# Performance work log

Measured on AMD Instinct MI355X. Metric: run time of the kernel, lower is better.

Reference implementation:

```python
import jax, jax.numpy as jnp
import numpy as np

N_NODES = 50000
IN_CH, HID_CH, OUT_CH = 128, 128, 64
N_EDGES = 800000


def setup_inputs() -> dict:
    key = jax.random.key(0)
    k = jax.random.split(key, 6)
    x = jax.random.normal(k[0], (N_NODES, IN_CH), dtype=jnp.float32)
    edge_index = jax.random.randint(k[1], (2, N_EDGES), 0, N_NODES, dtype=jnp.int64)
    # Glorot-ish init for weights
    W1 = jax.random.normal(k[2], (IN_CH, HID_CH), dtype=jnp.float32) * (1.0 / np.sqrt(IN_CH))
    b1 = jnp.zeros((HID_CH,), dtype=jnp.float32)
    W2 = jax.random.normal(k[3], (HID_CH, OUT_CH), dtype=jnp.float32) * (1.0 / np.sqrt(HID_CH))
    b2 = jnp.zeros((OUT_CH,), dtype=jnp.float32)
    return {"x": x, "edge_index": edge_index, "W1": W1, "b1": b1, "W2": W2, "b2": b2}


def _gcn_conv(x, src, dst, W, b, n_nodes):
    """PyG GCNConv: linear, add self-loops, symmetric deg^-1/2 normalization, scatter-add."""
    h = x @ W  # [N, F_out]
    loop = jnp.arange(n_nodes, dtype=src.dtype)
    s = jnp.concatenate([src, loop])  # [E+N]
    d = jnp.concatenate([dst, loop])
    # in-degree on target nodes (including self-loops), edge weight = 1
    deg = jnp.zeros((n_nodes,), dtype=h.dtype).at[d].add(1.0)
    dinv = jnp.where(deg > 0, jax.lax.rsqrt(deg), 0.0)
    norm = dinv[s] * dinv[d]  # [E+N]
    msg = h[s] * norm[:, None]  # [E+N, F_out]
    out = jax.ops.segment_sum(msg, d, num_segments=n_nodes)
    return out + b


def reference(x, edge_index, W1, b1, W2, b2):
    src, dst = edge_index[0], edge_index[1]
    h = _gcn_conv(x, src, dst, W1, b1, N_NODES)
    h = jax.nn.relu(h)
    # dropout in eval mode -> identity
    out = _gcn_conv(h, src, dst, W2, b2, N_NODES)
    return out
```

## Files before the change

### kernel.cpp

```cpp
#include <hip/hip_runtime.h>

typedef __attribute__((ext_vector_type(8))) short bf16x8;
typedef __attribute__((ext_vector_type(4))) float f32x4;

constexpr int NN = 50000;
constexpr int NE = 800000;
constexpr int C1 = 128;
constexpr int C2 = 64;
constexpr int NBK = 196;
constexpr int EPB = 2048;
constexpr int NBLK = (NE + EPB - 1) / EPB;
constexpr int MT = NN / 16;
constexpr int MMB = 250;
constexpr int MMWAVES = MMB * 4;

__device__ __forceinline__ unsigned short f2bf(float f) {
    unsigned int u = __float_as_uint(f);
    u += 0x7FFFu + ((u >> 16) & 1u);
    return (unsigned short)(u >> 16);
}
__device__ __forceinline__ float2 bf2f(unsigned int u) {
    return make_float2(__uint_as_float(u << 16), __uint_as_float(u & 0xFFFF0000u));
}
__device__ __forceinline__ bf16x8 pack8(float4 a, float4 b) {
    bf16x8 r;
    r[0] = (short)f2bf(a.x); r[1] = (short)f2bf(a.y);
    r[2] = (short)f2bf(a.z); r[3] = (short)f2bf(a.w);
    r[4] = (short)f2bf(b.x); r[5] = (short)f2bf(b.y);
    r[6] = (short)f2bf(b.z); r[7] = (short)f2bf(b.w);
    return r;
}

__global__ __launch_bounds__(256) void bin_kernel(const int* __restrict__ src,
                                                  const int* __restrict__ dst,
                                                  unsigned int* __restrict__ ebuf,
                                                  int* __restrict__ localOff,
                                                  int* __restrict__ bktHist) {
    __shared__ int lhist[NBK];
    __shared__ int ls[256];
    __shared__ int lcur[NBK];
    __shared__ unsigned int lbuf[EPB];
    const int t = threadIdx.x;
    const int base = blockIdx.x * EPB;
    if (t < NBK) lhist[t] = 0;
    __syncthreads();
    int b[8]; unsigned int p[8];
    #pragma unroll
    for (int i = 0; i < 8; i++) {
        int e = base + i * 256 + t;
        if (e < NE) {
            int s = src[e], d = dst[e];
            b[i] = d >> 8;
            p[i] = ((unsigned int)(d & 255) << 16) | (unsigned int)s;
            atomicAdd(&lhist[b[i]], 1);
        } else b[i] = -1;
    }
    __syncthreads();
    int v = (t < NBK) ? lhist[t] : 0;
    ls[t] = v;
    __syncthreads();
    #pragma unroll
    for (int d = 1; d < 256; d <<= 1) {
        int u = (t >= d) ? ls[t - d] : 0;
        __syncthreads();
        ls[t] += u;
        __syncthreads();
    }
    if (t < NBK) {
        int ex = ls[t] - v;
        lcur[t] = ex;
        localOff[blockIdx.x * 200 + t] = ex;
        if (v > 0) atomicAdd(&bktHist[t], v);
    }
    if (t == NBK - 1) localOff[blockIdx.x * 200 + NBK] = ls[t];
    __syncthreads();
    #pragma unroll
    for (int i = 0; i < 8; i++) {
        if (b[i] >= 0) {
            int lp = atomicAdd(&lcur[b[i]], 1);
            lbuf[lp] = p[i];
        }
    }
    __syncthreads();
    #pragma unroll
    for (int i = 0; i < 8; i++)
        ebuf[base + i * 256 + t] = lbuf[i * 256 + t];
}

__global__ void scanC_kernel(const int* __restrict__ bktHist, int* __restrict__ bktOff) {
    __shared__ int ls[256];
    int t = threadIdx.x;
    int v = (t < NBK) ? bktHist[t] : 0;
    ls[t] = v;
    __syncthreads();
    #pragma unroll
    for (int d = 1; d < 256; d <<= 1) {
        int u = (t >= d) ? ls[t - d] : 0;
        __syncthreads();
        ls[t] += u;
        __syncthreads();
    }
    if (t < NBK) bktOff[t] = ls[t] - v;
    if (t == 0) bktOff[NBK] = NE;
}

__global__ __launch_bounds__(256) void place_kernel(const unsigned int* __restrict__ ebuf,
                                                    const int* __restrict__ localOff,
                                                    const int* __restrict__ bktOff,
                                                    int* __restrict__ esrc,
                                                    int* __restrict__ cnt,
                                                    int* __restrict__ off,
                                                    float* __restrict__ dinv) {
    __shared__ int lhist[256];
    __shared__ int ls[256];
    __shared__ int lcur[256];
    const int t = threadIdx.x;
    const int bkt = blockIdx.x;
    const int node0 = bkt << 8;
    const int nnodes = min(256, NN - node0);
    lhist[t] = 0;
    __syncthreads();
    for (int j = t; j < NBLK; j += 256) {
        int s = localOff[j * 200 + bkt];
        int e = localOff[j * 200 + bkt + 1];
        const unsigned int* q = ebuf + j * EPB;
        for (int k = s; k < e; k++) atomicAdd(&lhist[q[k] >> 16], 1);
    }
    __syncthreads();
    int v = lhist[t];
    ls[t] = v;
    __syncthreads();
    #pragma unroll
    for (int d = 1; d < 256; d <<= 1) {
        int u = (t >= d) ? ls[t - d] : 0;
        __syncthreads();
        ls[t] += u;
        __syncthreads();
    }
    int ex = ls[t] - v;
    lcur[t] = ex;
    const int segBase = bktOff[bkt];
    if (t < nnodes) {
        cnt[node0 + t] = v;
        off[node0 + t] = segBase + ex;
        dinv[node0 + t] = rsqrtf((float)v + 1.0f);
    }
    __syncthreads();
    for (int j = t; j < NBLK; j += 256) {
        int s = localOff[j * 200 + bkt];
        int e = localOff[j * 200 + bkt + 1];
        const unsigned int* q = ebuf + j * EPB;
        for (int k = s; k < e; k++) {
            unsigned int pp = q[k];
            int lp = atomicAdd(&lcur[pp >> 16], 1);
            esrc[segBase + lp] = (int)(pp & 0xFFFFu);
        }
    }
}

__global__ __launch_bounds__(256, 2) void mm1_kernel(const float* __restrict__ x,
                                                     const float* __restrict__ W,
                                                     const float* __restrict__ dinv,
                                                     unsigned short* __restrict__ g1) {
    __shared__ unsigned short wl[4][8][64][8];
    const int t = threadIdx.x;
    for (int i = 0; i < 64; i++) {
        int idx = i * 256 + t;
        int k = idx >> 7, n = idx & 127;
        wl[k >> 5][n >> 4][((k >> 3) & 3) * 16 + (n & 15)][k & 7] = f2bf(W[idx]);
    }
    __syncthreads();
    const int lane = t & 63, lm = lane & 15, quad = lane >> 4;

    bf16x8 bfr[4][8];
    #pragma unroll
    for (int s = 0; s < 4; s++)
        #pragma unroll
        for (int nt = 0; nt < 8; nt++)
            bfr[s][nt] = *(const bf16x8*)&wl[s][nt][lane][0];

    int wg = blockIdx.x * 4 + (t >> 6);
    for (int tile = wg; tile < MT; tile += MMWAVES) {
        int row0 = tile << 4;
        const float* xr = x + (size_t)(row0 + lm) * 128 + quad * 8;
        bf16x8 af[4];
        #pragma unroll
        for (int s = 0; s < 4; s++) {
            float4 p = *(const float4*)(xr + s * 32);
            float4 q = *(const float4*)(xr + s * 32 + 4);
            af[s] = pack8(p, q);
        }
        f32x4 acc[8];
        #pragma unroll
        for (int nt = 0; nt < 8; nt++) acc[nt] = (f32x4){0.f, 0.f, 0.f, 0.f};
        #pragma unroll
        for (int s = 0; s < 4; s++)
            #pragma unroll
            for (int nt = 0; nt < 8; nt++)
                acc[nt] = __builtin_amdgcn_mfma_f32_16x16x32_bf16(af[s], bfr[s][nt],
                                                                  acc[nt], 0, 0, 0);
        float4 dv = *(const float4*)(dinv + row0 + quad * 4);
        float dvv[4] = {dv.x, dv.y, dv.z, dv.w};
        #pragma unroll
        for (int nt = 0; nt < 8; nt++)
            #pragma unroll
            for (int r = 0; r < 4; r++)
                g1[(size_t)(row0 + quad * 4 + r) * 128 + nt * 16 + lm] =
                    f2bf(acc[nt][r] * dvv[r]);
    }
}

__global__ __launch_bounds__(256, 2) void mm2_kernel(const unsigned short* __restrict__ x2,
                                                     const float* __restrict__ W,
                                                     const float* __restrict__ dinv,
                                                     unsigned short* __restrict__ g2) {
    __shared__ unsigned short wl[4][4][64][8];
    const int t = threadIdx.x;
    for (int i = 0; i < 32; i++) {
        int idx = i * 256 + t;
        int k = idx >> 6, n = idx & 63;
        wl[k >> 5][n >> 4][((k >> 3) & 3) * 16 + (n & 15)][k & 7] = f2bf(W[idx]);
    }
    __syncthreads();
    const int lane = t & 63, lm = lane & 15, quad = lane >> 4;

    bf16x8 bfr[4][4];
    #pragma unroll
    for (int s = 0; s < 4; s++)
        #pragma unroll
        for (int nt = 0; nt < 4; nt++)
            bfr[s][nt] = *(const bf16x8*)&wl[s][nt][lane][0];

    int wg = blockIdx.x * 4 + (t >> 6);
    for (int tile = wg; tile < MT; tile += MMWAVES) {
        int row0 = tile << 4;
        const bf16x8* xr = (const bf16x8*)(x2 + (size_t)(row0 + lm) * 128 + quad * 8);
        bf16x8 af[4];
        #pragma unroll
        for (int s = 0; s < 4; s++) af[s] = xr[s * 4];
        f32x4 acc[4];
        #pragma unroll
        for (int nt = 0; nt < 4; nt++) acc[nt] = (f32x4){0.f, 0.f, 0.f, 0.f};
        #pragma unroll
        for (int s = 0; s < 4; s++)
            #pragma unroll
            for (int nt = 0; nt < 4; nt++)
                acc[nt] = __builtin_amdgcn_mfma_f32_16x16x32_bf16(af[s], bfr[s][nt],
                                                                  acc[nt], 0, 0, 0);
        float4 dv = *(const float4*)(dinv + row0 + quad * 4);
        float dvv[4] = {dv.x, dv.y, dv.z, dv.w};
        #pragma unroll
        for (int nt = 0; nt < 4; nt++)
            #pragma unroll
            for (int r = 0; r < 4; r++)
                g2[(size_t)(row0 + quad * 4 + r) * 64 + nt * 16 + lm] =
                    f2bf(acc[nt][r] * dvv[r]);
    }
}

__global__ __launch_bounds__(256) void gather1_kernel(const unsigned int* __restrict__ g1,
                                                      const int* __restrict__ esrc,
                                                      const int* __restrict__ off,
                                                      const int* __restrict__ cnt,
                                                      const float* __restrict__ dinv,
                                                      const float* __restrict__ b1,
                                                      unsigned int* __restrict__ x2) {
    int wave = threadIdx.x >> 6;
    int lane = threadIdx.x & 63;
    int n = blockIdx.x * 4 + wave;
    if (n >= NN) return;
    float2 a0 = bf2f(g1[(size_t)n * 64 + lane]);
    float2 a1 = make_float2(0.f, 0.f);
    float2 a2 = make_float2(0.f, 0.f);
    float2 a3 = make_float2(0.f, 0.f);
    int s0 = off[n];
    int e0 = s0 + cnt[n];
    int i = s0;
    for (; i + 3 < e0; i += 4) {
        int sa = esrc[i], sb = esrc[i + 1], sc = esrc[i + 2], sd = esrc[i + 3];
        float2 va = bf2f(g1[(size_t)sa * 64 + lane]);
        float2 vb = bf2f(g1[(size_t)sb * 64 + lane]);
        float2 vc = bf2f(g1[(size_t)sc * 64 + lane]);
        float2 vd = bf2f(g1[(size_t)sd * 64 + lane]);
        a0.x += va.x; a0.y += va.y;
        a1.x += vb.x; a1.y += vb.y;
        a2.x += vc.x; a2.y += vc.y;
        a3.x += vd.x; a3.y += vd.y;
    }
    for (; i < e0; i++) {
        float2 va = bf2f(g1[(size_t)esrc[i] * 64 + lane]);
        a0.x += va.x; a0.y += va.y;
    }
    a0.x += a1.x + a2.x + a3.x;
    a0.y += a1.y + a2.y + a3.y;
    float s = dinv[n];
    float2 bb = ((const float2*)b1)[lane];
    float ox = fmaxf(s * a0.x + bb.x, 0.f);
    float oy = fmaxf(s * a0.y + bb.y, 0.f);
    x2[(size_t)n * 64 + lane] = ((unsigned int)f2bf(oy) << 16) | f2bf(ox);
}

__global__ __launch_bounds__(256) void gather2_kernel(const unsigned int* __restrict__ g2,
                                                      const int* __restrict__ esrc,
                                                      const int* __restrict__ off,
                                                      const int* __restrict__ cnt,
                                                      const float* __restrict__ dinv,
                                                      const float* __restrict__ b2,
                                                      float* __restrict__ out) {
    int lane = threadIdx.x & 31;
    int n = blockIdx.x * 8 + (threadIdx.x >> 5);
    if (n >= NN) return;
    float2 a0 = bf2f(g2[(size_t)n * 32 + lane]);
    float2 a1 = make_float2(0.f, 0.f);
    float2 a2 = make_float2(0.f, 0.f);
    float2 a3 = make_float2(0.f, 0.f);
    int s0 = off[n];
    int e0 = s0 + cnt[n];
    int i = s0;
    for (; i + 3 < e0; i += 4) {
        int sa = esrc[i], sb = esrc[i + 1], sc = esrc[i + 2], sd = esrc[i + 3];
        float2 va = bf2f(g2[(size_t)sa * 32 + lane]);
        float2 vb = bf2f(g2[(size_t)sb * 32 + lane]);
        float2 vc = bf2f(g2[(size_t)sc * 32 + lane]);
        float2 vd = bf2f(g2[(size_t)sd * 32 + lane]);
        a0.x += va.x; a0.y += va.y;
        a1.x += vb.x; a1.y += vb.y;
        a2.x += vc.x; a2.y += vc.y;
        a3.x += vd.x; a3.y += vd.y;
    }
    for (; i < e0; i++) {
        float2 va = bf2f(g2[(size_t)esrc[i] * 32 + lane]);
        a0.x += va.x; a0.y += va.y;
    }
    a0.x += a1.x + a2.x + a3.x;
    a0.y += a1.y + a2.y + a3.y;
    float s = dinv[n];
    float2 bb = ((const float2*)b2)[lane];
    ((float2*)out)[(size_t)n * 32 + lane] =
        make_float2(s * a0.x + bb.x, s * a0.y + bb.y);
}

extern "C" void kernel_launch(void* const* d_in, const int* in_sizes, int n_in,
                              void* d_out, int out_size, void* d_ws, size_t ws_size,
                              hipStream_t stream) {
    const float* x  = (const float*)d_in[0];
    const int* edges = (const int*)d_in[1];
    const float* W1 = (const float*)d_in[2];
    const float* b1 = (const float*)d_in[3];
    const float* W2 = (const float*)d_in[4];
    const float* b2 = (const float*)d_in[5];
    const int* src = edges;
    const int* dst = edges + NE;

    int* bktHist   = (int*)d_ws;
    int* bktOff    = bktHist + 200;
    int* localOff  = bktOff + 208;
    unsigned int* ebuf = (unsigned int*)(localOff + 78208);
    int* esrc      = (int*)(ebuf + (size_t)NBLK * EPB);
    int* cnt       = esrc + NE;
    int* off       = cnt + 50048;
    float* dinv    = (float*)(off + 50048);
    unsigned short* g1 = (unsigned short*)(dinv + 50048);
    unsigned short* x2 = g1 + (size_t)NN * C1;
    unsigned short* g2 = g1;
    float* out = (float*)d_out;

    hipMemsetAsync(bktHist, 0, 200 * sizeof(int), stream);

    bin_kernel<<<NBLK, 256, 0, stream>>>(src, dst, ebuf, localOff, bktHist);
    scanC_kernel<<<1, 256, 0, stream>>>(bktHist, bktOff);
    place_kernel<<<NBK, 256, 0, stream>>>(ebuf, localOff, bktOff, esrc, cnt, off, dinv);

    mm1_kernel<<<MMB, 256, 0, stream>>>(x, W1, dinv, g1);
    gather1_kernel<<<(NN + 3) / 4, 256, 0, stream>>>((const unsigned int*)g1, esrc, off, cnt,
                                                     dinv, b1, (unsigned int*)x2);

    mm2_kernel<<<MMB, 256, 0, stream>>>(x2, W2, dinv, g2);
    gather2_kernel<<<(NN + 7) / 8, 256, 0, stream>>>((const unsigned int*)g2, esrc, off, cnt,
                                                     dinv, b2, out);
}
```

Measured before the change: 211.6 us.

## Split gather across column groups with edge-parallel lanes, fold scan into place, 16-bit edge sources

Each gather kernel now splits the feature columns into groups of 8 bf16 pairs per block. The 8 sub-lanes of each column stride over a node's edges in parallel and combine their partial sums with xor shuffles, so each destination node's neighbour loads are spread across the wave instead of issued sequentially per node. The bucket prefix scan moves into place_kernel, which removes one kernel launch, and edge source indices are stored as 16-bit values to halve index traffic. Each gather row read now fetches only 32 bytes per column group, which may lower coalescing efficiency. Every place block also recomputes the same small scan redundantly.

```diff
diff --git a/kernel.cpp b/kernel.cpp
--- a/kernel.cpp
+++ b/kernel.cpp
@@ -87,37 +87,32 @@
         ebuf[base + i * 256 + t] = lbuf[i * 256 + t];
 }
 
-__global__ void scanC_kernel(const int* __restrict__ bktHist, int* __restrict__ bktOff) {
-    __shared__ int ls[256];
-    int t = threadIdx.x;
-    int v = (t < NBK) ? bktHist[t] : 0;
-    ls[t] = v;
-    __syncthreads();
-    #pragma unroll
-    for (int d = 1; d < 256; d <<= 1) {
-        int u = (t >= d) ? ls[t - d] : 0;
-        __syncthreads();
-        ls[t] += u;
-        __syncthreads();
-    }
-    if (t < NBK) bktOff[t] = ls[t] - v;
-    if (t == 0) bktOff[NBK] = NE;
-}
-
 __global__ __launch_bounds__(256) void place_kernel(const unsigned int* __restrict__ ebuf,
                                                     const int* __restrict__ localOff,
-                                                    const int* __restrict__ bktOff,
-                                                    int* __restrict__ esrc,
+                                                    const int* __restrict__ bktHist,
+                                                    unsigned short* __restrict__ esrc,
                                                     int* __restrict__ cnt,
                                                     int* __restrict__ off,
                                                     float* __restrict__ dinv) {
     __shared__ int lhist[256];
     __shared__ int ls[256];
     __shared__ int lcur[256];
+    __shared__ int sSegBase;
     const int t = threadIdx.x;
     const int bkt = blockIdx.x;
     const int node0 = bkt << 8;
     const int nnodes = min(256, NN - node0);
+    int v0 = (t < NBK) ? bktHist[t] : 0;
+    ls[t] = v0;
+    __syncthreads();
+    #pragma unroll
+    for (int d = 1; d < 256; d <<= 1) {
+        int u = (t >= d) ? ls[t - d] : 0;
+        __syncthreads();
+        ls[t] += u;
+        __syncthreads();
+    }
+    if (t == bkt) sSegBase = ls[t] - v0;
     lhist[t] = 0;
     __syncthreads();
     for (int j = t; j < NBLK; j += 256) {
@@ -139,7 +134,7 @@
     }
     int ex = ls[t] - v;
     lcur[t] = ex;
-    const int segBase = bktOff[bkt];
+    const int segBase = sSegBase;
     if (t < nnodes) {
         cnt[node0 + t] = v;
         off[node0 + t] = segBase + ex;
@@ -153,7 +148,7 @@
         for (int k = s; k < e; k++) {
             unsigned int pp = q[k];
             int lp = atomicAdd(&lcur[pp >> 16], 1);
-            esrc[segBase + lp] = (int)(pp & 0xFFFFu);
+            esrc[segBase + lp] = (unsigned short)(pp & 0xFFFFu);
         }
     }
 }
@@ -259,85 +254,74 @@
 }
 
 __global__ __launch_bounds__(256) void gather1_kernel(const unsigned int* __restrict__ g1,
-                                                      const int* __restrict__ esrc,
+                                                      const unsigned short* __restrict__ esrc,
                                                       const int* __restrict__ off,
                                                       const int* __restrict__ cnt,
                                                       const float* __restrict__ dinv,
                                                       const float* __restrict__ b1,
                                                       unsigned int* __restrict__ x2) {
-    int wave = threadIdx.x >> 6;
-    int lane = threadIdx.x & 63;
-    int n = blockIdx.x * 4 + wave;
-    if (n >= NN) return;
-    float2 a0 = bf2f(g1[(size_t)n * 64 + lane]);
-    float2 a1 = make_float2(0.f, 0.f);
-    float2 a2 = make_float2(0.f, 0.f);
-    float2 a3 = make_float2(0.f, 0.f);
-    int s0 = off[n];
-    int e0 = s0 + cnt[n];
-    int i = s0;
-    for (; i + 3 < e0; i += 4) {
-        int sa = esrc[i], sb = esrc[i + 1], sc = esrc[i + 2], sd = esrc[i + 3];
-        float2 va = bf2f(g1[(size_t)sa * 64 + lane]);
-        float2 vb = bf2f(g1[(size_t)sb * 64 + lane]);
-        float2 vc = bf2f(g1[(size_t)sc * 64 + lane]);
-        float2 vd = bf2f(g1[(size_t)sd * 64 + lane]);
-        a0.x += va.x; a0.y += va.y;
-        a1.x += vb.x; a1.y += vb.y;
-        a2.x += vc.x; a2.y += vc.y;
-        a3.x += vd.x; a3.y += vd.y;
-    }
-    for (; i < e0; i++) {
-        float2 va = bf2f(g1[(size_t)esrc[i] * 64 + lane]);
-        a0.x += va.x; a0.y += va.y;
-    }
-    a0.x += a1.x + a2.x + a3.x;
-    a0.y += a1.y + a2.y + a3.y;
-    float s = dinv[n];
-    float2 bb = ((const float2*)b1)[lane];
-    float ox = fmaxf(s * a0.x + bb.x, 0.f);
-    float oy = fmaxf(s * a0.y + bb.y, 0.f);
-    x2[(size_t)n * 64 + lane] = ((unsigned int)f2bf(oy) << 16) | f2bf(ox);
+    const int cg = blockIdx.x & 7;
+    const int nb = blockIdx.x >> 3;
+    const int wave = threadIdx.x >> 6, lane = threadIdx.x & 63;
+    const int sub = lane >> 3, cp = lane & 7;
+    const int col = cg * 8 + cp;
+    #pragma unroll
+    for (int ni = 0; ni < 4; ni++) {
+        int n = nb * 16 + wave * 4 + ni;
+        int s0 = off[n], c = cnt[n];
+        float2 a = make_float2(0.f, 0.f);
+        if (sub == 0) a = bf2f(g1[(size_t)n * 64 + col]);
+        for (int i = sub; i < c; i += 8) {
+            int s = esrc[s0 + i];
+            float2 v = bf2f(g1[(size_t)s * 64 + col]);
+            a.x += v.x; a.y += v.y;
+        }
+        a.x += __shfl_xor(a.x, 8);  a.y += __shfl_xor(a.y, 8);
+        a.x += __shfl_xor(a.x, 16); a.y += __shfl_xor(a.y, 16);
+        a.x += __shfl_xor(a.x, 32); a.y += __shfl_xor(a.y, 32);
+        if (sub == 0) {
+            float s = dinv[n];
+            float2 bb = ((const float2*)b1)[col];
+            float ox = fmaxf(s * a.x + bb.x, 0.f);
+            float oy = fmaxf(s * a.y + bb.y, 0.f);
+            x2[(size_t)n * 64 + col] = ((unsigned int)f2bf(oy) << 16) | f2bf(ox);
+        }
+    }
 }
 
 __global__ __launch_bounds__(256) void gather2_kernel(const unsigned int* __restrict__ g2,
-                                                      const int* __restrict__ esrc,
+                                                      const unsigned short* __restrict__ esrc,
                                                       const int* __restrict__ off,
                                                       const int* __restrict__ cnt,
                                                       const float* __restrict__ dinv,
                                                       const float* __restrict__ b2,
                                                       float* __restrict__ out) {
-    int lane = threadIdx.x & 31;
-    int n = blockIdx.x * 8 + (threadIdx.x >> 5);
-    if (n >= NN) return;
-    float2 a0 = bf2f(g2[(size_t)n * 32 + lane]);
-    float2 a1 = make_float2(0.f, 0.f);
-    float2 a2 = make_float2(0.f, 0.f);
-    float2 a3 = make_float2(0.f, 0.f);
-    int s0 = off[n];
-    int e0 = s0 + cnt[n];
-    int i = s0;
-    for (; i + 3 < e0; i += 4) {
-        int sa = esrc[i], sb = esrc[i + 1], sc = esrc[i + 2], sd = esrc[i + 3];
-        float2 va = bf2f(g2[(size_t)sa * 32 + lane]);
-        float2 vb = bf2f(g2[(size_t)sb * 32 + lane]);
-        float2 vc = bf2f(g2[(size_t)sc * 32 + lane]);
-        float2 vd = bf2f(g2[(size_t)sd * 32 + lane]);
-        a0.x += va.x; a0.y += va.y;
-        a1.x += vb.x; a1.y += vb.y;
-        a2.x += vc.x; a2.y += vc.y;
-        a3.x += vd.x; a3.y += vd.y;
-    }
-    for (; i < e0; i++) {
-        float2 va = bf2f(g2[(size_t)esrc[i] * 32 + lane]);
-        a0.x += va.x; a0.y += va.y;
-    }
-    a0.x += a1.x + a2.x + a3.x;
-    a0.y += a1.y + a2.y + a3.y;
-    float s = dinv[n];
-    float2 bb = ((const float2*)b2)[lane];
-    ((float2*)out)[(size_t)n * 32 + lane] =
-        make_float2(s * a0.x + bb.x, s * a0.y + bb.y);
+    const int cg = blockIdx.x & 3;
+    const int nb = blockIdx.x >> 2;
+    const int wave = threadIdx.x >> 6, lane = threadIdx.x & 63;
+    const int sub = lane >> 3, cp = lane & 7;
+    const int col = cg * 8 + cp;
+    #pragma unroll
+    for (int ni = 0; ni < 4; ni++) {
+        int n = nb * 16 + wave * 4 + ni;
+        int s0 = off[n], c = cnt[n];
+        float2 a = make_float2(0.f, 0.f);
+        if (sub == 0) a = bf2f(g2[(size_t)n * 32 + col]);
+        for (int i = sub; i < c; i += 8) {
+            int s = esrc[s0 + i];
+            float2 v = bf2f(g2[(size_t)s * 32 + col]);
+            a.x += v.x; a.y += v.y;
+        }
+        a.x += __shfl_xor(a.x, 8);  a.y += __shfl_xor(a.y, 8);
+        a.x += __shfl_xor(a.x, 16); a.y += __shfl_xor(a.y, 16);
+        a.x += __shfl_xor(a.x, 32); a.y += __shfl_xor(a.y, 32);
+        if (sub == 0) {
+            float s = dinv[n];
+            float2 bb = ((const float2*)b2)[col];
+            ((float2*)out)[(size_t)n * 32 + col] =
+                make_float2(s * a.x + bb.x, s * a.y + bb.y);
+        }
+    }
 }
 
 extern "C" void kernel_launch(void* const* d_in, const int* in_sizes, int n_in,
@@ -353,11 +337,10 @@
     const int* dst = edges + NE;
 
     int* bktHist   = (int*)d_ws;
-    int* bktOff    = bktHist + 200;
-    int* localOff  = bktOff + 208;
+    int* localOff  = bktHist + 208;
     unsigned int* ebuf = (unsigned int*)(localOff + 78208);
-    int* esrc      = (int*)(ebuf + (size_t)NBLK * EPB);
-    int* cnt       = esrc + NE;
+    unsigned short* esrc = (unsigned short*)(ebuf + (size_t)NBLK * EPB);
+    int* cnt       = (int*)(esrc + 800768);
     int* off       = cnt + 50048;
     float* dinv    = (float*)(off + 50048);
     unsigned short* g1 = (unsigned short*)(dinv + 50048);
@@ -368,14 +351,13 @@
     hipMemsetAsync(bktHist, 0, 200 * sizeof(int), stream);
 
     bin_kernel<<<NBLK, 256, 0, stream>>>(src, dst, ebuf, localOff, bktHist);
-    scanC_kernel<<<1, 256, 0, stream>>>(bktHist, bktOff);
-    place_kernel<<<NBK, 256, 0, stream>>>(ebuf, localOff, bktOff, esrc, cnt, off, dinv);
+    place_kernel<<<NBK, 256, 0, stream>>>(ebuf, localOff, bktHist, esrc, cnt, off, dinv);
 
     mm1_kernel<<<MMB, 256, 0, stream>>>(x, W1, dinv, g1);
-    gather1_kernel<<<(NN + 3) / 4, 256, 0, stream>>>((const unsigned int*)g1, esrc, off, cnt,
-                                                     dinv, b1, (unsigned int*)x2);
+    gather1_kernel<<<MT * 8, 256, 0, stream>>>((const unsigned int*)g1, esrc, off, cnt,
+                                               dinv, b1, (unsigned int*)x2);
 
     mm2_kernel<<<MMB, 256, 0, stream>>>(x2, W2, dinv, g2);
-    gather2_kernel<<<(NN + 7) / 8, 256, 0, stream>>>((const unsigned int*)g2, esrc, off, cnt,
-                                                     dinv, b2, out);
-}
+    gather2_kernel<<<MT * 4, 256, 0, stream>>>((const unsigned int*)g2, esrc, off, cnt,
+                                               dinv, b2, out);
+}
```

After: 335.1 us. +58.3%, slower.
